# Performance work log

Measured on AMD Instinct MI355X. Metric: run time of the kernel, lower is better.

The kernel has to match this reference:

```python
import jax, jax.numpy as jnp
import numpy as np

FULL_SCALE = 128
TOPK = 8
R = 0.5


def setup_inputs() -> dict:
    key = jax.random.key(0)
    ks = jax.random.split(key, 6)
    B, Na, Nb, D = 4, 8192, 8192, 256
    return {
        "a_feats": jax.random.normal(ks[0], (B, Na, D), jnp.float32),
        "b_feats": jax.random.normal(ks[1], (B, Nb, D), jnp.float32),
        "coords_a": jax.random.randint(ks[2], (B, Na, 3), 0, 2048, jnp.int32),
        "coords_b": jax.random.randint(ks[3], (B, Nb, 3), 0, 2048, jnp.int32),
        "w1": jax.random.normal(ks[4], (D, 2 * D), jnp.float32) / np.sqrt(2 * D),
        "b1": jnp.zeros((D,), jnp.float32),
        "w2": jax.random.normal(ks[5], (D, D), jnp.float32) / np.sqrt(D),
        "b2": jnp.zeros((D,), jnp.float32),
    }


def _cli_one(af, bf, ca, cb, w1, b1, w2, b2):
    # af:[Na,D] bf:[Nb,D] ca:[Na,3] cb:[Nb,3] (float coords, already //16)
    # torch.cdist (euclidean) / full_scale
    d2 = (jnp.sum(ca * ca, 1)[:, None] + jnp.sum(cb * cb, 1)[None, :]
          - 2.0 * ca @ cb.T)
    dist = jnp.sqrt(jnp.maximum(d2, 0.0)) / FULL_SCALE  # [Na, Nb]
    neg_d, idx = jax.lax.top_k(-dist, TOPK)             # smallest k distances
    dw = R - jnp.clip(-neg_d, 0.0, R)                   # [Na, k]
    nb = bf[idx]                                        # gather [Na, k, D]
    x = jnp.concatenate([nb, af[:, None, :] - nb], axis=-1)  # [Na, k, 2D]
    h = jax.nn.relu(jnp.einsum('nkf,df->nkd', x, w1) + b1) * dw[..., None]
    o = jnp.einsum('nkd,ed->nke', h, w2) + b2           # [Na, k, D]
    return jnp.sum(o, axis=1)                           # [Na, D]


def reference(a_feats, b_feats, coords_a, coords_b, w1, b1, w2, b2):
    ca = (coords_a // 16).astype(jnp.float32)
    cb = (coords_b // 16).astype(jnp.float32)
    fuse = jax.vmap(lambda af, bf, x, y: _cli_one(af, bf, x, y, w1, b1, w2, b2))(
        a_feats, b_feats, ca, cb)
    # ME.cat(a, tmp): concatenate features along channel dim
    return jnp.concatenate([a_feats, fuse], axis=-1)  # [B, Na, 2D]
```

## Files before the change

### kernel.cpp

```cpp
#include <hip/hip_runtime.h>
#include <math.h>

typedef short short8_t __attribute__((ext_vector_type(8)));
typedef __bf16 bf16x8_t __attribute__((ext_vector_type(8)));
typedef float f32x4_t __attribute__((ext_vector_type(4)));

__device__ __forceinline__ float bf2f(unsigned short u) {
  unsigned v = ((unsigned)u) << 16;
  return __builtin_bit_cast(float, v);
}
__device__ __forceinline__ unsigned short f2bf(float f) {
  unsigned x = __builtin_bit_cast(unsigned, f);
  x += 0x7fffu + ((x >> 16) & 1u);
  return (unsigned short)(x >> 16);
}

#define NA 8192
#define NB 8192
#define NBATCH 4
#define DIM 256
#define NPTS (NBATCH * NA)
#define NCELL 2048
#define SUBL 8

__device__ __forceinline__ void kins(unsigned k[8], unsigned x) {
  unsigned c = x < k[7] ? x : k[7];
#pragma unroll
  for (int i = 6; i >= 0; i--) {
    unsigned hi = k[i] > c ? k[i] : c;
    c = k[i] < c ? k[i] : c;
    k[i + 1] = hi;
  }
  k[0] = c;
}

__global__ __launch_bounds__(256) void prep_weights(
    const float* __restrict__ w1, const float* __restrict__ w2,
    unsigned short* __restrict__ Wdiff, unsigned short* __restrict__ Wb,
    unsigned short* __restrict__ W2b) {
  int d = blockIdx.x, t = threadIdx.x;
  float wa = w1[d * 512 + t];
  float wb = w1[d * 512 + 256 + t];
  Wdiff[d * 256 + t] = f2bf(wa - wb);
  Wb[d * 256 + t] = f2bf(wb);
  W2b[d * 256 + t] = f2bf(w2[d * 256 + t]);
}

__global__ __launch_bounds__(256) void zero_counts(
    unsigned* __restrict__ bcnt, unsigned* __restrict__ acnt,
    unsigned* __restrict__ failcnt) {
  int i = blockIdx.x * 256 + threadIdx.x;
  bcnt[i] = 0;
  acnt[i] = 0;
  if (i == 0) *failcnt = 0;
}

__global__ __launch_bounds__(256) void pack_count(
    const int* __restrict__ coords, unsigned* __restrict__ pk,
    unsigned* __restrict__ cnt) {
  int i = blockIdx.x * 256 + threadIdx.x;
  int x = (coords[(size_t)i * 3 + 0] >> 4) & 127;
  int y = (coords[(size_t)i * 3 + 1] >> 4) & 127;
  int z = (coords[(size_t)i * 3 + 2] >> 4) & 127;
  pk[i] = (unsigned)(x | (y << 7) | (z << 14));
  int cid = ((i >> 13) << 9) | ((x >> 4) << 6) | ((y >> 4) << 3) | (z >> 4);
  atomicAdd(cnt + cid, 1u);
}

__global__ __launch_bounds__(256) void scan_cells(
    const unsigned* __restrict__ bcnt, const unsigned* __restrict__ acnt,
    unsigned* __restrict__ boff, unsigned* __restrict__ aoff,
    unsigned* __restrict__ bcur, unsigned* __restrict__ acur) {
  __shared__ unsigned p[256];
  const int t = threadIdx.x;
  for (int tab = 0; tab < 2; tab++) {
    const unsigned* cnt = tab ? acnt : bcnt;
    unsigned* off = tab ? aoff : boff;
    unsigned* cur = tab ? acur : bcur;
    unsigned loc[8], sum = 0;
#pragma unroll
    for (int k = 0; k < 8; k++) { loc[k] = sum; sum += cnt[t * 8 + k]; }
    p[t] = sum;
    __syncthreads();
    for (int d = 1; d < 256; d <<= 1) {
      unsigned v = (t >= d) ? p[t - d] : 0u;
      __syncthreads();
      p[t] += v;
      __syncthreads();
    }
    unsigned base = (t == 0) ? 0u : p[t - 1];
#pragma unroll
    for (int k = 0; k < 8; k++) {
      unsigned o = base + loc[k];
      off[t * 8 + k] = o;
      cur[t * 8 + k] = o;
    }
    if (t == 255) off[2048] = base + sum;
    __syncthreads();
  }
}

__global__ __launch_bounds__(256) void scatter_pts(
    const unsigned* __restrict__ pk, unsigned* __restrict__ cur,
    uint2* __restrict__ out) {
  int i = blockIdx.x * 256 + threadIdx.x;
  unsigned v = pk[i];
  int cx = (v & 127) >> 4, cy = ((v >> 7) & 127) >> 4, cz = ((v >> 14) & 127) >> 4;
  int cid = ((i >> 13) << 9) | (cx << 6) | (cy << 3) | cz;
  unsigned pos = atomicAdd(cur + cid, 1u);
  out[pos] = make_uint2(v, (unsigned)(i & 8191));
}

#define LDT 72
template <int F32IN>
__global__ __launch_bounds__(512) void gemm_wide(
    const void* __restrict__ Ain, const short* __restrict__ W,
    float* __restrict__ Cf, unsigned short* __restrict__ Cb,
    const float* __restrict__ bias, float bias_scale,
    int c_stride, int c_coloff, float* __restrict__ copyout) {
  __shared__ __attribute__((aligned(16))) short As[128 * LDT];
  __shared__ __attribute__((aligned(16))) short Bs[256 * LDT];
  const int tid = threadIdx.x;
  const int row0 = blockIdx.x * 128;
  const int w = tid >> 6, lane = tid & 63;
  const int wm = (w & 1) * 64, wn = (w >> 1) * 64;
  f32x4_t acc[4][4] = {};
  for (int k0 = 0; k0 < 256; k0 += 64) {
    if (F32IN) {
      const float* Af = (const float*)Ain;
#pragma unroll
      for (int i = 0; i < 2; i++) {
        int c = tid + 512 * i;
        int r = c >> 3, kc = (c & 7) * 8;
        const float* src = Af + (size_t)(row0 + r) * 256 + k0 + kc;
        float4 v0 = *(const float4*)src;
        float4 v1 = *(const float4*)(src + 4);
        short8_t vb;
        vb[0] = (short)f2bf(v0.x); vb[1] = (short)f2bf(v0.y);
        vb[2] = (short)f2bf(v0.z); vb[3] = (short)f2bf(v0.w);
        vb[4] = (short)f2bf(v1.x); vb[5] = (short)f2bf(v1.y);
        vb[6] = (short)f2bf(v1.z); vb[7] = (short)f2bf(v1.w);
        *(short8_t*)(As + r * LDT + kc) = vb;
        if (copyout) {
          float4* dst = (float4*)(copyout + (size_t)(row0 + r) * 512 + k0 + kc);
          dst[0] = v0;
          dst[1] = v1;
        }
      }
    } else {
      const short* Ab = (const short*)Ain;
#pragma unroll
      for (int i = 0; i < 2; i++) {
        int c = tid + 512 * i;
        int r = c >> 3, kc = (c & 7) * 8;
        *(short8_t*)(As + r * LDT + kc) =
            *(const short8_t*)(Ab + (size_t)(row0 + r) * 256 + k0 + kc);
      }
    }
#pragma unroll
    for (int i = 0; i < 4; i++) {
      int c = tid + 512 * i;
      int r = c >> 3, kc = (c & 7) * 8;
      *(short8_t*)(Bs + r * LDT + kc) =
          *(const short8_t*)(W + (size_t)r * 256 + k0 + kc);
    }
    __syncthreads();
#pragma unroll
    for (int kk = 0; kk < 64; kk += 32) {
      const int kof = kk + (lane >> 4) * 8;
      bf16x8_t af[4], bfr[4];
#pragma unroll
      for (int i = 0; i < 4; i++) {
        af[i] = __builtin_bit_cast(bf16x8_t,
            *(const short8_t*)(As + (wm + i * 16 + (lane & 15)) * LDT + kof));
        bfr[i] = __builtin_bit_cast(bf16x8_t,
            *(const short8_t*)(Bs + (wn + i * 16 + (lane & 15)) * LDT + kof));
      }
#pragma unroll
      for (int i = 0; i < 4; i++)
#pragma unroll
        for (int j = 0; j < 4; j++)
          acc[i][j] = __builtin_amdgcn_mfma_f32_16x16x32_bf16(
              af[i], bfr[j], acc[i][j], 0, 0, 0);
    }
    __syncthreads();
  }
#pragma unroll
  for (int i = 0; i < 4; i++) {
    int row = row0 + wm + i * 16 + ((lane >> 4) * 4);
#pragma unroll
    for (int j = 0; j < 4; j++) {
      int col = wn + j * 16 + (lane & 15);
      float bv = bias ? bias[col] * bias_scale : 0.f;
#pragma unroll
      for (int r = 0; r < 4; r++) {
        float v = acc[i][j][r] + bv;
        size_t off = (size_t)(row + r) * c_stride + c_coloff + col;
        if (Cf) Cf[off] = v;
        else Cb[off] = f2bf(v);
      }
    }
  }
}

__global__ __launch_bounds__(256) void topk_bins(
    const unsigned* __restrict__ boff, const uint2* __restrict__ bcj,
    const uint2* __restrict__ acj, int* __restrict__ idxb,
    float* __restrict__ dwb, unsigned* __restrict__ failcnt,
    unsigned* __restrict__ faillist) {
  const int tid = blockIdx.x * 256 + threadIdx.x;
  const int t = tid / SUBL;
  const int sub = tid & (SUBL - 1);
  const uint2 av = acj[t];
  const int batch = t >> 13;
  const int ax = av.x & 127, ay = (av.x >> 7) & 127, az = (av.x >> 14) & 127;
  const int cx = ax >> 4, cy = ay >> 4, cz = az >> 4;
  const int xlo = max(cx - 1, 0), xhi = min(cx + 1, 7);
  const int ylo = max(cy - 1, 0), yhi = min(cy + 1, 7);
  const int zlo = max(cz - 1, 0), zhi1 = min(cz + 1, 7) + 1;
  unsigned k[8];
#pragma unroll
  for (int s = 0; s < 8; s++) k[s] = 0xFFFFFFF8u + s;
  for (int nx = xlo; nx <= xhi; nx++) {
    for (int ny = ylo; ny <= yhi; ny++) {
      const int cb = (batch << 9) | (nx << 6) | (ny << 3);
      const int gs = (int)boff[cb + zlo];
      const int ge = (int)boff[cb + zhi1];
      for (int i = gs + sub; i < ge; i += SUBL) {
        const uint2 b = bcj[i];
        const int dx = ax - (int)(b.x & 127);
        const int dy = ay - (int)((b.x >> 7) & 127);
        const int dz = az - (int)((b.x >> 14) & 127);
        const unsigned d2 = (unsigned)(__mul24(dx, dx) + __mul24(dy, dy) +
                                       __mul24(dz, dz));
        kins(k, (d2 << 13) | b.y);
      }
    }
  }
  const int lane = threadIdx.x & 63;
#pragma unroll
  for (int half = 1; half < SUBL; half <<= 1) {
    unsigned o[8];
#pragma unroll
    for (int s = 0; s < 8; s++)
      o[s] = (unsigned)__shfl((int)k[s], lane ^ half, 64);
#pragma unroll
    for (int s = 0; s < 8; s++) kins(k, o[s]);
  }
  if (sub == 0) {
    const int g = (batch << 13) | (int)av.y;
#pragma unroll
    for (int s = 0; s < 8; s++) {
      unsigned key = k[s];
      idxb[(size_t)g * 8 + s] = (int)(key & 8191u);
      float dist = sqrtf((float)(key >> 13)) * (1.0f / 128.0f);
      dwb[(size_t)g * 8 + s] = 0.5f - fminf(dist, 0.5f);
    }
    if (k[7] >= (289u << 13)) {
      unsigned fp = atomicAdd(failcnt, 1u);
      faillist[fp] = (unsigned)g;
    }
  }
}

__global__ __launch_bounds__(256) void topk_fallback(
    const unsigned* __restrict__ failcnt, const unsigned* __restrict__ faillist,
    const uint2* __restrict__ bcj, const unsigned* __restrict__ apk,
    int* __restrict__ idxb, float* __restrict__ dwb) {
  __shared__ unsigned sk[4 * 8];
  const int tid = threadIdx.x;
  const int wv = tid >> 6, lane = tid & 63;
  const unsigned nf = *failcnt;
  for (unsigned fi = blockIdx.x; fi < nf; fi += gridDim.x) {
    const unsigned g = faillist[fi];
    const int batch = (int)(g >> 13);
    const unsigned av = apk[g];
    const int ax = av & 127, ay = (av >> 7) & 127, az = (av >> 14) & 127;
    const uint2* pb = bcj + ((size_t)batch << 13);
    unsigned k[8];
#pragma unroll
    for (int s = 0; s < 8; s++) k[s] = 0xFFFFFFF8u + s;
#pragma unroll 8
    for (int i = tid; i < NB; i += 256) {
      const uint2 b = pb[i];
      const int dx = ax - (int)(b.x & 127);
      const int dy = ay - (int)((b.x >> 7) & 127);
      const int dz = az - (int)((b.x >> 14) & 127);
      const unsigned d2 = (unsigned)(__mul24(dx, dx) + __mul24(dy, dy) +
                                     __mul24(dz, dz));
      kins(k, (d2 << 13) | b.y);
    }
#pragma unroll
    for (int half = 32; half >= 1; half >>= 1) {
      unsigned o[8];
#pragma unroll
      for (int s = 0; s < 8; s++)
        o[s] = (unsigned)__shfl((int)k[s], lane ^ half, 64);
#pragma unroll
      for (int s = 0; s < 8; s++) kins(k, o[s]);
    }
    if (lane == 0) {
#pragma unroll
      for (int s = 0; s < 8; s++) sk[wv * 8 + s] = k[s];
    }
    __syncthreads();
    if (tid == 0) {
#pragma unroll
      for (int w = 1; w < 4; w++)
#pragma unroll
        for (int s = 0; s < 8; s++) kins(k, sk[w * 8 + s]);
#pragma unroll
      for (int s = 0; s < 8; s++) {
        unsigned key = k[s];
        idxb[(size_t)g * 8 + s] = (int)(key & 8191u);
        float dist = sqrtf((float)(key >> 13)) * (1.0f / 128.0f);
        dwb[(size_t)g * 8 + s] = 0.5f - fminf(dist, 0.5f);
      }
    }
    __syncthreads();
  }
}

__global__ __launch_bounds__(256) void fuse_kernel(
    const unsigned short* __restrict__ Pa, const unsigned short* __restrict__ Pb,
    const int* __restrict__ idxb, const float* __restrict__ dwb,
    unsigned short* __restrict__ H) {
  const int g = blockIdx.x * 4 + (threadIdx.x >> 6);
  const int lane = threadIdx.x & 63;
  const int batch = g >> 13;
  const size_t fo = (size_t)g * 256 + lane * 4;
  ushort4 pav = *(const ushort4*)(Pa + fo);
  const float pa0 = bf2f(pav.x), pa1 = bf2f(pav.y), pa2 = bf2f(pav.z),
              pa3 = bf2f(pav.w);
  float h0 = 0.f, h1 = 0.f, h2 = 0.f, h3 = 0.f;
  const size_t bbase = (size_t)(batch << 13) * 256;
#pragma unroll
  for (int k = 0; k < 8; k++) {
    const int j = idxb[(size_t)g * 8 + k];
    const float w = dwb[(size_t)g * 8 + k];
    const ushort4 pbv =
        *(const ushort4*)(Pb + bbase + (size_t)j * 256 + lane * 4);
    h0 += fmaxf(pa0 + bf2f(pbv.x), 0.f) * w;
    h1 += fmaxf(pa1 + bf2f(pbv.y), 0.f) * w;
    h2 += fmaxf(pa2 + bf2f(pbv.z), 0.f) * w;
    h3 += fmaxf(pa3 + bf2f(pbv.w), 0.f) * w;
  }
  ushort4 hv;
  hv.x = f2bf(h0); hv.y = f2bf(h1); hv.z = f2bf(h2); hv.w = f2bf(h3);
  *(ushort4*)(H + fo) = hv;
}

extern "C" void kernel_launch(void* const* d_in, const int* in_sizes, int n_in,
                              void* d_out, int out_size, void* d_ws,
                              size_t ws_size, hipStream_t stream) {
  const float* a_feats = (const float*)d_in[0];
  const float* b_feats = (const float*)d_in[1];
  const int* coords_a = (const int*)d_in[2];
  const int* coords_b = (const int*)d_in[3];
  const float* w1 = (const float*)d_in[4];
  const float* b1 = (const float*)d_in[5];
  const float* w2 = (const float*)d_in[6];
  const float* b2 = (const float*)d_in[7];
  float* outp = (float*)d_out;

  char* p = (char*)d_ws;
  auto take = [&](size_t bytes) {
    char* r = p;
    p += (bytes + 255) & ~(size_t)255;
    return r;
  };
  unsigned short* Pa = (unsigned short*)take((size_t)NPTS * DIM * 2);
  unsigned short* Pb = (unsigned short*)take((size_t)NPTS * DIM * 2);
  unsigned short* Hb = (unsigned short*)take((size_t)NPTS * DIM * 2);
  int* idxb = (int*)take((size_t)NPTS * 8 * 4);
  float* dwb = (float*)take((size_t)NPTS * 8 * 4);
  unsigned* bpk = (unsigned*)take((size_t)NPTS * 4);
  unsigned* apk = (unsigned*)take((size_t)NPTS * 4);
  unsigned* bcnt = (unsigned*)take(NCELL * 4);
  unsigned* acnt = (unsigned*)take(NCELL * 4);
  unsigned* bcur = (unsigned*)take(NCELL * 4);
  unsigned* acur = (unsigned*)take(NCELL * 4);
  unsigned* boff = (unsigned*)take((NCELL + 1) * 4);
  unsigned* aoff = (unsigned*)take((NCELL + 1) * 4);
  uint2* bcj = (uint2*)take((size_t)NPTS * 8);
  uint2* acj = (uint2*)take((size_t)NPTS * 8);
  unsigned* failcnt = (unsigned*)take(256);
  unsigned* faillist = (unsigned*)take((size_t)NPTS * 4);
  unsigned short* Wdiff = (unsigned short*)take(256 * 256 * 2);
  unsigned short* Wb16 = (unsigned short*)take(256 * 256 * 2);
  unsigned short* W2b = (unsigned short*)take(256 * 256 * 2);

  prep_weights<<<256, 256, 0, stream>>>(w1, w2, Wdiff, Wb16, W2b);

  zero_counts<<<NCELL / 256, 256, 0, stream>>>(bcnt, acnt, failcnt);
  pack_count<<<NPTS / 256, 256, 0, stream>>>(coords_b, bpk, bcnt);
  pack_count<<<NPTS / 256, 256, 0, stream>>>(coords_a, apk, acnt);
  scan_cells<<<1, 256, 0, stream>>>(bcnt, acnt, boff, aoff, bcur, acur);
  scatter_pts<<<NPTS / 256, 256, 0, stream>>>(bpk, bcur, bcj);
  scatter_pts<<<NPTS / 256, 256, 0, stream>>>(apk, acur, acj);

  gemm_wide<1><<<NPTS / 128, 512, 0, stream>>>(
      (const void*)a_feats, (const short*)Wb16, nullptr, Pa, b1, 1.0f, 256, 0,
      outp);
  gemm_wide<1><<<NPTS / 128, 512, 0, stream>>>(
      (const void*)b_feats, (const short*)Wdiff, nullptr, Pb, nullptr, 0.0f,
      256, 0, nullptr);

  topk_bins<<<NPTS * SUBL / 256, 256, 0, stream>>>(boff, bcj, acj, idxb, dwb,
                                                   failcnt, faillist);
  topk_fallback<<<256, 256, 0, stream>>>(failcnt, faillist, bcj, apk, idxb,
                                         dwb);

  fuse_kernel<<<NPTS / 4, 256, 0, stream>>>(Pa, Pb, idxb, dwb, Hb);

  gemm_wide<0><<<NPTS / 128, 512, 0, stream>>>(
      (const void*)Hb, (const short*)W2b, outp, nullptr, b2, 8.0f, 512, 256,
      nullptr);
}
```

Measured before the change: 246.2 us.

## Fuse neighbor gather-relu-sum into second GEMM and merge small prep kernels

The separate fuse_kernel that built the hidden tensor H in global memory is removed. The final GEMM now gathers the neighbor Pb rows, applies relu and the distance weights, and writes bf16 directly into its shared-memory A tile. This drops a full write and read of H. The zero-count kernel is folded into prep_weights, and the a/b pack and scatter launches are merged into single launches, which cuts launch count. In exchange the GEMM A-tile load now does 8 scattered gathers per element chunk with no overlap, and it adds shared-memory arrays that may lower occupancy.

Measured after the change: 239.1 us. 2.9% less time.

```diff
diff --git a/kernel.cpp b/kernel.cpp
--- a/kernel.cpp
+++ b/kernel.cpp
@@ -37,28 +37,32 @@
 __global__ __launch_bounds__(256) void prep_weights(
     const float* __restrict__ w1, const float* __restrict__ w2,
     unsigned short* __restrict__ Wdiff, unsigned short* __restrict__ Wb,
-    unsigned short* __restrict__ W2b) {
+    unsigned short* __restrict__ W2b, unsigned* __restrict__ bcnt,
+    unsigned* __restrict__ acnt, unsigned* __restrict__ failcnt) {
   int d = blockIdx.x, t = threadIdx.x;
   float wa = w1[d * 512 + t];
   float wb = w1[d * 512 + 256 + t];
   Wdiff[d * 256 + t] = f2bf(wa - wb);
   Wb[d * 256 + t] = f2bf(wb);
   W2b[d * 256 + t] = f2bf(w2[d * 256 + t]);
-}
-
-__global__ __launch_bounds__(256) void zero_counts(
-    unsigned* __restrict__ bcnt, unsigned* __restrict__ acnt,
-    unsigned* __restrict__ failcnt) {
-  int i = blockIdx.x * 256 + threadIdx.x;
-  bcnt[i] = 0;
-  acnt[i] = 0;
-  if (i == 0) *failcnt = 0;
-}
-
-__global__ __launch_bounds__(256) void pack_count(
-    const int* __restrict__ coords, unsigned* __restrict__ pk,
-    unsigned* __restrict__ cnt) {
-  int i = blockIdx.x * 256 + threadIdx.x;
+  if (d < 8) {
+    int i = d * 256 + t;
+    bcnt[i] = 0;
+    acnt[i] = 0;
+    if (i == 0) *failcnt = 0;
+  }
+}
+
+__global__ __launch_bounds__(256) void pack_count_ab(
+    const int* __restrict__ coords_b, const int* __restrict__ coords_a,
+    unsigned* __restrict__ bpk, unsigned* __restrict__ apk,
+    unsigned* __restrict__ bcnt, unsigned* __restrict__ acnt) {
+  int gi = blockIdx.x * 256 + threadIdx.x;
+  const int isA = gi >= NPTS;
+  const int i = gi & (NPTS - 1);
+  const int* __restrict__ coords = isA ? coords_a : coords_b;
+  unsigned* __restrict__ pk = isA ? apk : bpk;
+  unsigned* __restrict__ cnt = isA ? acnt : bcnt;
   int x = (coords[(size_t)i * 3 + 0] >> 4) & 127;
   int y = (coords[(size_t)i * 3 + 1] >> 4) & 127;
   int z = (coords[(size_t)i * 3 + 2] >> 4) & 127;
@@ -100,10 +104,16 @@
   }
 }
 
-__global__ __launch_bounds__(256) void scatter_pts(
-    const unsigned* __restrict__ pk, unsigned* __restrict__ cur,
-    uint2* __restrict__ out) {
-  int i = blockIdx.x * 256 + threadIdx.x;
+__global__ __launch_bounds__(256) void scatter_ab(
+    const unsigned* __restrict__ bpk, const unsigned* __restrict__ apk,
+    unsigned* __restrict__ bcur, unsigned* __restrict__ acur,
+    uint2* __restrict__ bout, uint2* __restrict__ aout) {
+  int gi = blockIdx.x * 256 + threadIdx.x;
+  const int isA = gi >= NPTS;
+  const int i = gi & (NPTS - 1);
+  const unsigned* __restrict__ pk = isA ? apk : bpk;
+  unsigned* __restrict__ cur = isA ? acur : bcur;
+  uint2* __restrict__ out = isA ? aout : bout;
   unsigned v = pk[i];
   int cx = (v & 127) >> 4, cy = ((v >> 7) & 127) >> 4, cz = ((v >> 14) & 127) >> 4;
   int cid = ((i >> 13) << 9) | (cx << 6) | (cy << 3) | cz;
@@ -112,21 +122,36 @@
 }
 
 #define LDT 72
-template <int F32IN>
+template <int MODE>
 __global__ __launch_bounds__(512) void gemm_wide(
     const void* __restrict__ Ain, const short* __restrict__ W,
     float* __restrict__ Cf, unsigned short* __restrict__ Cb,
     const float* __restrict__ bias, float bias_scale,
-    int c_stride, int c_coloff, float* __restrict__ copyout) {
+    int c_stride, int c_coloff, float* __restrict__ copyout,
+    const unsigned short* __restrict__ Pb, const int* __restrict__ idxb,
+    const float* __restrict__ dwb) {
   __shared__ __attribute__((aligned(16))) short As[128 * LDT];
   __shared__ __attribute__((aligned(16))) short Bs[256 * LDT];
+  __shared__ int sIdx[128 * 8];
+  __shared__ float sDw[128 * 8];
   const int tid = threadIdx.x;
   const int row0 = blockIdx.x * 128;
   const int w = tid >> 6, lane = tid & 63;
   const int wm = (w & 1) * 64, wn = (w >> 1) * 64;
   f32x4_t acc[4][4] = {};
+  if (MODE == 2) {
+#pragma unroll
+    for (int q = 0; q < 2; q++) {
+      int ii = tid * 2 + q;
+      int r = ii >> 3, s = ii & 7;
+      sIdx[ii] = idxb[(size_t)(row0 + r) * 8 + s];
+      sDw[ii] = dwb[(size_t)(row0 + r) * 8 + s];
+    }
+    __syncthreads();
+  }
+  const size_t bbase256 = MODE == 2 ? ((size_t)(row0 >> 13) << 13) * 256 : 0;
   for (int k0 = 0; k0 < 256; k0 += 64) {
-    if (F32IN) {
+    if (MODE == 1) {
       const float* Af = (const float*)Ain;
 #pragma unroll
       for (int i = 0; i < 2; i++) {
@@ -148,13 +173,39 @@
         }
       }
     } else {
-      const short* Ab = (const short*)Ain;
+      const unsigned short* Pa = (const unsigned short*)Ain;
 #pragma unroll
       for (int i = 0; i < 2; i++) {
         int c = tid + 512 * i;
         int r = c >> 3, kc = (c & 7) * 8;
-        *(short8_t*)(As + r * LDT + kc) =
-            *(const short8_t*)(Ab + (size_t)(row0 + r) * 256 + k0 + kc);
+        const int row = row0 + r;
+        const unsigned short* pap = Pa + (size_t)row * 256 + k0 + kc;
+        ushort4 pa0 = *(const ushort4*)pap;
+        ushort4 pa1 = *(const ushort4*)(pap + 4);
+        float paf[8] = {bf2f(pa0.x), bf2f(pa0.y), bf2f(pa0.z), bf2f(pa0.w),
+                        bf2f(pa1.x), bf2f(pa1.y), bf2f(pa1.z), bf2f(pa1.w)};
+        float h[8] = {};
+#pragma unroll
+        for (int k = 0; k < 8; k++) {
+          const int j = sIdx[r * 8 + k];
+          const float wk = sDw[r * 8 + k];
+          const unsigned short* pbp =
+              Pb + bbase256 + (size_t)j * 256 + k0 + kc;
+          ushort4 pb0 = *(const ushort4*)pbp;
+          ushort4 pb1 = *(const ushort4*)(pbp + 4);
+          h[0] += fmaxf(paf[0] + bf2f(pb0.x), 0.f) * wk;
+          h[1] += fmaxf(paf[1] + bf2f(pb0.y), 0.f) * wk;
+          h[2] += fmaxf(paf[2] + bf2f(pb0.z), 0.f) * wk;
+          h[3] += fmaxf(paf[3] + bf2f(pb0.w), 0.f) * wk;
+          h[4] += fmaxf(paf[4] + bf2f(pb1.x), 0.f) * wk;
+          h[5] += fmaxf(paf[5] + bf2f(pb1.y), 0.f) * wk;
+          h[6] += fmaxf(paf[6] + bf2f(pb1.z), 0.f) * wk;
+          h[7] += fmaxf(paf[7] + bf2f(pb1.w), 0.f) * wk;
+        }
+        short8_t vb;
+#pragma unroll
+        for (int m = 0; m < 8; m++) vb[m] = (short)f2bf(h[m]);
+        *(short8_t*)(As + r * LDT + kc) = vb;
       }
     }
 #pragma unroll
@@ -321,35 +372,6 @@
   }
 }
 
-__global__ __launch_bounds__(256) void fuse_kernel(
-    const unsigned short* __restrict__ Pa, const unsigned short* __restrict__ Pb,
-    const int* __restrict__ idxb, const float* __restrict__ dwb,
-    unsigned short* __restrict__ H) {
-  const int g = blockIdx.x * 4 + (threadIdx.x >> 6);
-  const int lane = threadIdx.x & 63;
-  const int batch = g >> 13;
-  const size_t fo = (size_t)g * 256 + lane * 4;
-  ushort4 pav = *(const ushort4*)(Pa + fo);
-  const float pa0 = bf2f(pav.x), pa1 = bf2f(pav.y), pa2 = bf2f(pav.z),
-              pa3 = bf2f(pav.w);
-  float h0 = 0.f, h1 = 0.f, h2 = 0.f, h3 = 0.f;
-  const size_t bbase = (size_t)(batch << 13) * 256;
-#pragma unroll
-  for (int k = 0; k < 8; k++) {
-    const int j = idxb[(size_t)g * 8 + k];
-    const float w = dwb[(size_t)g * 8 + k];
-    const ushort4 pbv =
-        *(const ushort4*)(Pb + bbase + (size_t)j * 256 + lane * 4);
-    h0 += fmaxf(pa0 + bf2f(pbv.x), 0.f) * w;
-    h1 += fmaxf(pa1 + bf2f(pbv.y), 0.f) * w;
-    h2 += fmaxf(pa2 + bf2f(pbv.z), 0.f) * w;
-    h3 += fmaxf(pa3 + bf2f(pbv.w), 0.f) * w;
-  }
-  ushort4 hv;
-  hv.x = f2bf(h0); hv.y = f2bf(h1); hv.z = f2bf(h2); hv.w = f2bf(h3);
-  *(ushort4*)(H + fo) = hv;
-}
-
 extern "C" void kernel_launch(void* const* d_in, const int* in_sizes, int n_in,
                               void* d_out, int out_size, void* d_ws,
                               size_t ws_size, hipStream_t stream) {
@@ -371,7 +393,6 @@
   };
   unsigned short* Pa = (unsigned short*)take((size_t)NPTS * DIM * 2);
   unsigned short* Pb = (unsigned short*)take((size_t)NPTS * DIM * 2);
-  unsigned short* Hb = (unsigned short*)take((size_t)NPTS * DIM * 2);
   int* idxb = (int*)take((size_t)NPTS * 8 * 4);
   float* dwb = (float*)take((size_t)NPTS * 8 * 4);
   unsigned* bpk = (unsigned*)take((size_t)NPTS * 4);
@@ -390,30 +411,27 @@
   unsigned short* Wb16 = (unsigned short*)take(256 * 256 * 2);
   unsigned short* W2b = (unsigned short*)take(256 * 256 * 2);
 
-  prep_weights<<<256, 256, 0, stream>>>(w1, w2, Wdiff, Wb16, W2b);
-
-  zero_counts<<<NCELL / 256, 256, 0, stream>>>(bcnt, acnt, failcnt);
-  pack_count<<<NPTS / 256, 256, 0, stream>>>(coords_b, bpk, bcnt);
-  pack_count<<<NPTS / 256, 256, 0, stream>>>(coords_a, apk, acnt);
+  prep_weights<<<256, 256, 0, stream>>>(w1, w2, Wdiff, Wb16, W2b, bcnt, acnt,
+                                        failcnt);
+  pack_count_ab<<<2 * NPTS / 256, 256, 0, stream>>>(coords_b, coords_a, bpk,
+                                                    apk, bcnt, acnt);
   scan_cells<<<1, 256, 0, stream>>>(bcnt, acnt, boff, aoff, bcur, acur);
-  scatter_pts<<<NPTS / 256, 256, 0, stream>>>(bpk, bcur, bcj);
-  scatter_pts<<<NPTS / 256, 256, 0, stream>>>(apk, acur, acj);
+  scatter_ab<<<2 * NPTS / 256, 256, 0, stream>>>(bpk, apk, bcur, acur, bcj,
+                                                 acj);
 
   gemm_wide<1><<<NPTS / 128, 512, 0, stream>>>(
       (const void*)a_feats, (const short*)Wb16, nullptr, Pa, b1, 1.0f, 256, 0,
-      outp);
+      outp, nullptr, nullptr, nullptr);
   gemm_wide<1><<<NPTS / 128, 512, 0, stream>>>(
       (const void*)b_feats, (const short*)Wdiff, nullptr, Pb, nullptr, 0.0f,
-      256, 0, nullptr);
+      256, 0, nullptr, nullptr, nullptr, nullptr);
 
   topk_bins<<<NPTS * SUBL / 256, 256, 0, stream>>>(boff, bcj, acj, idxb, dwb,
                                                    failcnt, faillist);
   topk_fallback<<<256, 256, 0, stream>>>(failcnt, faillist, bcj, apk, idxb,
                                          dwb);
 
-  fuse_kernel<<<NPTS / 4, 256, 0, stream>>>(Pa, Pb, idxb, dwb, Hb);
-
-  gemm_wide<0><<<NPTS / 128, 512, 0, stream>>>(
-      (const void*)Hb, (const short*)W2b, outp, nullptr, b2, 8.0f, 512, 256,
-      nullptr);
-}
+  gemm_wide<2><<<NPTS / 128, 512, 0, stream>>>(
+      (const void*)Pa, (const short*)W2b, outp, nullptr, b2, 8.0f, 512, 256,
+      nullptr, Pb, idxb, dwb);
+}
```
